# Kernel optimization log

Hardware: AMD Instinct MI355X
Metric: run time of the kernel (lower is better)

The kernel has to match this reference:

```python
import jax, jax.numpy as jnp
import numpy as np

W_SIZE = 16
WIN = 2 * W_SIZE + 1
OUT_F = 256
MODEL = 512  # output_features * 2


def setup_inputs() -> dict:
    key = jax.random.key(0)
    ks = jax.random.split(key, 7)
    B, T = 4, 2048
    s = 0.02
    return {
        "x": jax.random.normal(ks[0], (B, T, MODEL), jnp.float32),
        "encoder_outputs": jax.random.normal(ks[1], (B, T, OUT_F), jnp.float32),
        # Attention: attn Linear (OUT_F + MODEL -> OUT_F), v Linear (OUT_F -> 1, no bias)
        "W_attn": jax.random.normal(ks[2], (OUT_F + MODEL, OUT_F), jnp.float32) * s,
        "b_attn": jnp.zeros((OUT_F,), jnp.float32),
        "v": jax.random.normal(ks[3], (OUT_F,), jnp.float32) * s,
        # final linear: (MODEL + OUT_F -> OUT_F)
        "W_lin": jax.random.normal(ks[4], (MODEL + OUT_F, OUT_F), jnp.float32) * s,
        "b_lin": jnp.zeros((OUT_F,), jnp.float32),
    }


def _windows(enc):
    B, T, F = enc.shape
    padded = jnp.pad(enc, ((0, 0), (W_SIZE, W_SIZE), (0, 0)))
    idx = jnp.arange(T)[:, None] + jnp.arange(WIN)[None, :]
    return padded[:, idx]


def reference(x, encoder_outputs, W_attn, b_attn, v, W_lin, b_lin):
    win = _windows(encoder_outputs)
    B, T, W, F = win.shape
    # additive (Bahdanau) score: concat(hidden, window) -> Linear -> tanh -> v
    Wh, We = W_attn[:MODEL], W_attn[MODEL:]
    energy = jnp.tanh(
        jnp.einsum('btm,mo->bto', x, Wh)[:, :, None, :]
        + jnp.einsum('btwf,fo->btwo', win, We)
        + b_attn
    )
    scores = jnp.einsum('btwo,o->btw', energy, v)
    a = jax.nn.softmax(scores, axis=-1)
    weighted = jnp.einsum('btw,btwf->btf', a, win)        # [B, T, F]
    h = jnp.concatenate([x, weighted], axis=-1)           # [B, T, MODEL+F]
    out = jax.nn.sigmoid(jnp.einsum('btk,ko->bto', h, W_lin) + b_lin)
    return out, a[:, :, None, :]
```

## Files before the change

kernel.cpp:

```cpp
#include <hip/hip_runtime.h>
#include <math.h>

#define T_DIM 2048
#define B_DIM 4
#define BT (B_DIM * T_DIM)
#define MODEL 512
#define OUTF 256
#define WSZ 16
#define WIN 33

#define BM 128
#define BN 64
#define BK 32

#define TB 16
#define HALO 48
#define EP 264

#define ESCALE 2.885390081777927f
#define ECLAMP 30.0f

typedef __attribute__((ext_vector_type(8))) short bf16x8;
typedef __attribute__((ext_vector_type(4))) float f32x4;

__device__ inline unsigned short f2bf(float f) {
  unsigned int u = __float_as_uint(f);
  u += 0x7fffu + ((u >> 16) & 1u);
  return (unsigned short)(u >> 16);
}
__device__ inline float bflo(unsigned int u) {
  return __uint_as_float(u << 16);
}
__device__ inline float bfhi(unsigned int u) {
  return __uint_as_float(u & 0xffff0000u);
}
__device__ inline float fast_sigmoid(float z) {
  return __builtin_amdgcn_rcpf(1.f + __expf(-z));
}

__global__ __launch_bounds__(256) void prepW_kernel(
    const float* __restrict__ W_attn, const float* __restrict__ W_lin,
    unsigned short* __restrict__ wtT, unsigned short* __restrict__ wlT) {
  const int bid = blockIdx.x, o = threadIdx.x;
  const float* W = (bid < 96) ? W_attn : W_lin;
  unsigned short* WT = (bid < 96) ? wtT : wlT;
  const int k0 = ((bid < 96) ? bid : bid - 96) * 8;
  unsigned short t[8];
#pragma unroll
  for (int j = 0; j < 8; ++j) t[j] = f2bf(W[(k0 + j) * OUTF + o]);
  *(uint4*)&WT[o * 768 + k0] = *(const uint4*)t;
}

template <int KS, int MODE>
__device__ __forceinline__ void gemm_body(
    unsigned short (*As)[BM * 40], unsigned short (*Bs)[BN * 40], int rb,
    const float* __restrict__ A, int lda,
    const unsigned short* __restrict__ wtT,
    const unsigned short* __restrict__ wlT,
    const float* __restrict__ b_attn, const float* __restrict__ b_lin,
    unsigned short* __restrict__ outb, float* __restrict__ outf,
    unsigned short* __restrict__ encb) {
  const int tid = threadIdx.x;
  const int cb = rb >> 6, rp = rb & 63;
  const int row0 = rp * BM;

  const unsigned short* Bt;
  int colg;
  if (MODE == 0) {
    Bt = (cb < 4) ? (wtT + (size_t)(cb * 64) * 768)
                  : (wlT + (size_t)((cb - 4) * 64) * 768);
    colg = (cb & 3) * 64;
  } else {
    Bt = wtT + (size_t)(cb * 64) * 768 + 512;
    colg = cb * 64;
  }

  const int arow = tid >> 2, akp = (tid & 3) * 8;
  const int bcol = tid >> 3, bkp = (tid & 7) * 4;
  const float* aptr = A + (size_t)(row0 + arow) * lda + akp;
  const unsigned short* bptr = Bt + (size_t)bcol * 768 + bkp;

  float4 ra0[2], ra1[2];
  uint2 rbv[2];
  auto LOADS = [&](int sl, int ks) {
    const float* ap = aptr + ks * BK;
    ra0[sl] = *(const float4*)ap;
    ra1[sl] = *(const float4*)(ap + 4);
    rbv[sl] = *(const uint2*)(bptr + ks * BK);
  };
  auto WRITE = [&](int sl, int buf, int ks) {
    unsigned short t[8] = {f2bf(ra0[sl].x), f2bf(ra0[sl].y), f2bf(ra0[sl].z),
                           f2bf(ra0[sl].w), f2bf(ra1[sl].x), f2bf(ra1[sl].y),
                           f2bf(ra1[sl].z), f2bf(ra1[sl].w)};
    *(uint4*)&As[buf][arow * 40 + akp] = *(const uint4*)t;
    *(uint2*)&Bs[buf][bcol * 40 + bkp] = rbv[sl];
    if (MODE == 1 && cb == 0)
      *(uint4*)&encb[(size_t)(row0 + arow) * OUTF + ks * BK + akp] =
          *(const uint4*)t;
  };

  const int w = tid >> 6, lane = tid & 63;
  const int lr = lane & 15, kg = lane >> 4;
  const int rbase = (w & 3) * 32;
  const int cbase = (w >> 2) * 32;

  f32x4 acc[2][2] = {{{0.f, 0.f, 0.f, 0.f}, {0.f, 0.f, 0.f, 0.f}},
                     {{0.f, 0.f, 0.f, 0.f}, {0.f, 0.f, 0.f, 0.f}}};

  LOADS(0, 0);
  if (KS > 1) LOADS(1, 1);
  WRITE(0, 0, 0);
  __syncthreads();

#pragma unroll
  for (int ks = 0; ks < KS; ++ks) {
    if (ks + 2 < KS) LOADS(ks & 1, ks + 2);
    const int bf = ks & 1;
    bf16x8 a0 = *(const bf16x8*)&As[bf][(rbase + lr) * 40 + kg * 8];
    bf16x8 a1 = *(const bf16x8*)&As[bf][(rbase + 16 + lr) * 40 + kg * 8];
    bf16x8 b0 = *(const bf16x8*)&Bs[bf][(cbase + lr) * 40 + kg * 8];
    bf16x8 b1 = *(const bf16x8*)&Bs[bf][(cbase + 16 + lr) * 40 + kg * 8];
    acc[0][0] = __builtin_amdgcn_mfma_f32_16x16x32_bf16(a0, b0, acc[0][0], 0, 0, 0);
    acc[0][1] = __builtin_amdgcn_mfma_f32_16x16x32_bf16(a0, b1, acc[0][1], 0, 0, 0);
    acc[1][0] = __builtin_amdgcn_mfma_f32_16x16x32_bf16(a1, b0, acc[1][0], 0, 0, 0);
    acc[1][1] = __builtin_amdgcn_mfma_f32_16x16x32_bf16(a1, b1, acc[1][1], 0, 0, 0);
    if (ks + 1 < KS) WRITE((ks + 1) & 1, (ks + 1) & 1, ks + 1);
    __syncthreads();
  }

#pragma unroll
  for (int m = 0; m < 2; ++m) {
#pragma unroll
    for (int f = 0; f < 2; ++f) {
      const int col = colg + cbase + f * 16 + lr;
#pragma unroll
      for (int r = 0; r < 4; ++r) {
        const int row = row0 + rbase + m * 16 + kg * 4 + r;
        float val = acc[m][f][r];
        if (MODE == 0) {
          if (cb < 4) {
            const float y = fminf((val + b_attn[col]) * ESCALE, ECLAMP);
            outb[(size_t)row * OUTF + col] =
                f2bf(__builtin_amdgcn_exp2f(y));
          } else {
            outf[(size_t)row * OUTF + col] = val + b_lin[col];
          }
        } else {
          const float y = fminf(val * ESCALE, ECLAMP);
          outb[(size_t)row * OUTF + col] = f2bf(__builtin_amdgcn_exp2f(y));
        }
      }
    }
  }
}

__global__ __launch_bounds__(512) void gemmAB_kernel(
    const float* __restrict__ x, const float* __restrict__ enc,
    const unsigned short* __restrict__ wtT,
    const unsigned short* __restrict__ wlT,
    const float* __restrict__ b_attn, const float* __restrict__ b_lin,
    unsigned short* __restrict__ xwe2, float* __restrict__ z1,
    unsigned short* __restrict__ ewe2, unsigned short* __restrict__ encb) {
  __shared__ unsigned short As[2][BM * 40];
  __shared__ unsigned short Bs[2][BN * 40];
  if (blockIdx.x < 512)
    gemm_body<16, 0>(As, Bs, blockIdx.x, x, MODEL, wtT, wlT, b_attn, b_lin,
                     xwe2, z1, nullptr);
  else
    gemm_body<8, 1>(As, Bs, blockIdx.x - 512, enc, OUTF, wtT, wlT, nullptr,
                    nullptr, ewe2, nullptr, encb);
}

__global__ __launch_bounds__(512) void attn_gemmc_kernel(
    const unsigned short* __restrict__ xwe2,
    const unsigned short* __restrict__ ewe2,
    const unsigned short* __restrict__ encb, const float* __restrict__ v,
    const unsigned short* __restrict__ wlT, const float* __restrict__ z1,
    float* __restrict__ out, float* __restrict__ a_out) {
  __shared__ unsigned short Ew[HALO * 256];
  __shared__ unsigned short Pw[TB * EP];

  const int tid = threadIdx.x;
  const int wv = tid >> 6, lane = tid & 63;
  const int rb = ((blockIdx.x & 7) << 6) | (blockIdx.x >> 3);
  const int t0 = rb * TB;
  const int b = t0 >> 11;
  const int tloc = t0 & (T_DIM - 1);
  const int g = lane >> 4, sl = lane & 15;

  for (int u = tid; u < HALO * 32; u += 512) {
    const int r = u >> 5, s = u & 31;
    const int tg = tloc - WSZ + r;
    uint4 q;
    if ((unsigned)tg < T_DIM)
      q = *(const uint4*)(ewe2 + (((size_t)(b * T_DIM + tg)) << 8) + s * 8);
    else
      q = make_uint4(0x3f803f80u, 0x3f803f80u, 0x3f803f80u, 0x3f803f80u);
    *(uint4*)&Ew[r * 256 + s * 8] = q;
  }

  float vf[16];
  {
    const float4* vp = (const float4*)(v + sl * 16);
#pragma unroll
    for (int j = 0; j < 4; ++j) {
      float4 t4 = vp[j];
      vf[4 * j] = t4.x; vf[4 * j + 1] = t4.y;
      vf[4 * j + 2] = t4.z; vf[4 * j + 3] = t4.w;
    }
  }
  __syncthreads();

  const int lrow = wv * 2;
  const int bt0 = t0 + lrow, bt1 = bt0 + 1;

  float xe0[16], xe1[16];
  {
    const uint4* xp0 = (const uint4*)(xwe2 + ((size_t)bt0 << 8) + sl * 16);
    const uint4* xp1 = (const uint4*)(xwe2 + ((size_t)bt1 << 8) + sl * 16);
    uint4 q0 = xp0[0], q1 = xp0[1], q2 = xp1[0], q3 = xp1[1];
    unsigned int u0[8] = {q0.x, q0.y, q0.z, q0.w, q1.x, q1.y, q1.z, q1.w};
    unsigned int u1[8] = {q2.x, q2.y, q2.z, q2.w, q3.x, q3.y, q3.z, q3.w};
#pragma unroll
    for (int j = 0; j < 8; ++j) {
      xe0[2 * j] = bflo(u0[j]); xe0[2 * j + 1] = bfhi(u0[j]);
      xe1[2 * j] = bflo(u1[j]); xe1[2 * j + 1] = bfhi(u1[j]);
    }
  }

  float s0 = 0.f, s1 = 0.f;
#pragma unroll
  for (int c = 0; c < 9; ++c) {
    const int w_ = c * 4 + g;
    const int rl0 = min(lrow + w_, HALO - 1);
    const int rl1 = min(lrow + 1 + w_, HALO - 1);
    const uint4 a0q = *(const uint4*)&Ew[rl0 * 256 + sl * 16];
    const uint4 a1q = *(const uint4*)&Ew[rl0 * 256 + sl * 16 + 8];
    const uint4 b0q = *(const uint4*)&Ew[rl1 * 256 + sl * 16];
    const uint4 b1q = *(const uint4*)&Ew[rl1 * 256 + sl * 16 + 8];
    unsigned int e0[8] = {a0q.x, a0q.y, a0q.z, a0q.w, a1q.x, a1q.y, a1q.z, a1q.w};
    unsigned int e1[8] = {b0q.x, b0q.y, b0q.z, b0q.w, b1q.x, b1q.y, b1q.z, b1q.w};
    float acc0 = 0.f, acc1 = 0.f;
#pragma unroll
    for (int j = 0; j < 8; ++j) {
      const float v0 = vf[2 * j], v1 = vf[2 * j + 1];
      const float vsj = v0 + v1;
      {
        const float E0 = xe0[2 * j] * bflo(e0[j]);
        const float E1 = xe0[2 * j + 1] * bfhi(e0[j]);
        const float den = (E0 + 1.f) * (E1 + 1.f);
        float num = fmaf(v0, E1, vsj);
        num = fmaf(v1, E0, num);
        acc0 = fmaf(num, __builtin_amdgcn_rcpf(den), acc0);
      }
      {
        const float E0 = xe1[2 * j] * bflo(e1[j]);
        const float E1 = xe1[2 * j + 1] * bfhi(e1[j]);
        const float den = (E0 + 1.f) * (E1 + 1.f);
        float num = fmaf(v0, E1, vsj);
        num = fmaf(v1, E0, num);
        acc1 = fmaf(num, __builtin_amdgcn_rcpf(den), acc1);
      }
    }
#pragma unroll
    for (int off = 1; off < 16; off <<= 1) {
      acc0 += __shfl_xor(acc0, off);
      acc1 += __shfl_xor(acc1, off);
    }
    const int src = (lane & 3) << 4;
    float c0v = __shfl(acc0, src), c1v = __shfl(acc1, src);
    if ((lane >> 2) == c) { s0 = c0v; s1 = c1v; }
  }

  float p0 = (lane < WIN) ? __builtin_amdgcn_exp2f(-ESCALE * s0) : 0.f;
  float p1 = (lane < WIN) ? __builtin_amdgcn_exp2f(-ESCALE * s1) : 0.f;
  float q0 = p0, q1 = p1;
#pragma unroll
  for (int off = 1; off < 64; off <<= 1) {
    q0 += __shfl_xor(q0, off);
    q1 += __shfl_xor(q1, off);
  }
  const float a0v = p0 * __builtin_amdgcn_rcpf(q0);
  const float a1v = p1 * __builtin_amdgcn_rcpf(q1);
  if (lane < WIN) {
    a_out[(size_t)bt0 * WIN + lane] = a0v;
    a_out[(size_t)bt1 * WIN + lane] = a1v;
  }

  {
    const int o4 = lane * 4;
    const int tbase = tloc + lrow - WSZ;
    float A0 = 0.f, A1 = 0.f, A2 = 0.f, A3 = 0.f;
    float B0 = 0.f, B1 = 0.f, B2 = 0.f, B3 = 0.f;
#pragma unroll
    for (int idx = 0; idx < WIN + 1; ++idx) {
      const int t2 = tbase + idx;
      const bool valid = ((unsigned)t2 < T_DIM);
      const int t2c = valid ? t2 : 0;
      const uint2 e2 =
          *(const uint2*)(encb + (((size_t)(b * T_DIM + t2c)) << 8) + o4);
      float aw0 = __shfl(a0v, idx & 63);
      float aw1 = __shfl(a1v, (idx - 1) & 63);
      aw0 = valid ? aw0 : 0.f;
      aw1 = valid ? aw1 : 0.f;
      const float f0 = bflo(e2.x), f1 = bfhi(e2.x);
      const float f2_ = bflo(e2.y), f3 = bfhi(e2.y);
      A0 = fmaf(aw0, f0, A0); B0 = fmaf(aw1, f0, B0);
      A1 = fmaf(aw0, f1, A1); B1 = fmaf(aw1, f1, B1);
      A2 = fmaf(aw0, f2_, A2); B2 = fmaf(aw1, f2_, B2);
      A3 = fmaf(aw0, f3, A3); B3 = fmaf(aw1, f3, B3);
    }
    uint2 pk;
    pk.x = (unsigned int)f2bf(A0) | ((unsigned int)f2bf(A1) << 16);
    pk.y = (unsigned int)f2bf(A2) | ((unsigned int)f2bf(A3) << 16);
    *(uint2*)&Pw[lrow * EP + o4] = pk;
    pk.x = (unsigned int)f2bf(B0) | ((unsigned int)f2bf(B1) << 16);
    pk.y = (unsigned int)f2bf(B2) | ((unsigned int)f2bf(B3) << 16);
    *(uint2*)&Pw[(lrow + 1) * EP + o4] = pk;
  }
  __syncthreads();

  const int lr = lane & 15, kg = lane >> 4;
  f32x4 acc[2] = {{0.f, 0.f, 0.f, 0.f}, {0.f, 0.f, 0.f, 0.f}};
#pragma unroll
  for (int kk = 0; kk < 8; ++kk) {
    bf16x8 a = *(const bf16x8*)&Pw[lr * EP + kk * 32 + kg * 8];
#pragma unroll
    for (int f = 0; f < 2; ++f) {
      const unsigned short* bp =
          wlT + (size_t)(wv * 32 + f * 16 + lr) * 768 + 512 + kk * 32 + kg * 8;
      acc[f] = __builtin_amdgcn_mfma_f32_16x16x32_bf16(
          a, *(const bf16x8*)bp, acc[f], 0, 0, 0);
    }
  }
#pragma unroll
  for (int f = 0; f < 2; ++f) {
    const int col = wv * 32 + f * 16 + lr;
#pragma unroll
    for (int r = 0; r < 4; ++r) {
      const int row = t0 + kg * 4 + r;
      out[(size_t)row * OUTF + col] =
          fast_sigmoid(acc[f][r] + z1[(size_t)row * OUTF + col]);
    }
  }
}

extern "C" void kernel_launch(void* const* d_in, const int* in_sizes, int n_in,
                              void* d_out, int out_size, void* d_ws,
                              size_t ws_size, hipStream_t stream) {
  const float* x      = (const float*)d_in[0];
  const float* enc    = (const float*)d_in[1];
  const float* W_attn = (const float*)d_in[2];
  const float* b_attn = (const float*)d_in[3];
  const float* v      = (const float*)d_in[4];
  const float* W_lin  = (const float*)d_in[5];
  const float* b_lin  = (const float*)d_in[6];

  float* out   = (float*)d_out;
  float* a_out = out + (size_t)BT * OUTF;

  unsigned short* wtT  = (unsigned short*)d_ws;
  unsigned short* wlT  = wtT + 768 * OUTF;
  unsigned short* xwe2 = wlT + 768 * OUTF;
  unsigned short* ewe2 = xwe2 + (size_t)BT * OUTF;
  float*          z1   = (float*)(ewe2 + (size_t)BT * OUTF);
  unsigned short* encb = (unsigned short*)(z1 + (size_t)BT * OUTF);

  prepW_kernel<<<192, 256, 0, stream>>>(W_attn, W_lin, wtT, wlT);
  gemmAB_kernel<<<768, 512, 0, stream>>>(x, enc, wtT, wlT, b_attn, b_lin,
                                         xwe2, z1, ewe2, encb);
  attn_gemmc_kernel<<<512, 512, 0, stream>>>(xwe2, ewe2, encb, v, wlT, z1,
                                             out, a_out);
}
```

Baseline: 53.38 us.

## Precompute enc@W_lin and apply attention weights as banded MFMA over window

Result: no change. 54.02 us (+1.2%).

```diff
diff --git a/kernel.cpp b/kernel.cpp
--- a/kernel.cpp
+++ b/kernel.cpp
@@ -15,7 +15,7 @@
 
 #define TB 16
 #define HALO 48
-#define EP 264
+#define TS 72
 
 #define ESCALE 2.885390081777927f
 #define ECLAMP 30.0f
@@ -59,21 +59,19 @@
     const unsigned short* __restrict__ wlT,
     const float* __restrict__ b_attn, const float* __restrict__ b_lin,
     unsigned short* __restrict__ outb, float* __restrict__ outf,
-    unsigned short* __restrict__ encb) {
+    unsigned short* __restrict__ outb2) {
   const int tid = threadIdx.x;
   const int cb = rb >> 6, rp = rb & 63;
   const int row0 = rp * BM;
 
   const unsigned short* Bt;
-  int colg;
-  if (MODE == 0) {
+  const int colg = (cb & 3) * 64;
+  if (MODE == 0)
     Bt = (cb < 4) ? (wtT + (size_t)(cb * 64) * 768)
                   : (wlT + (size_t)((cb - 4) * 64) * 768);
-    colg = (cb & 3) * 64;
-  } else {
-    Bt = wtT + (size_t)(cb * 64) * 768 + 512;
-    colg = cb * 64;
-  }
+  else
+    Bt = (cb < 4) ? (wtT + (size_t)(cb * 64) * 768 + 512)
+                  : (wlT + (size_t)((cb - 4) * 64) * 768 + 512);
 
   const int arow = tid >> 2, akp = (tid & 3) * 8;
   const int bcol = tid >> 3, bkp = (tid & 7) * 4;
@@ -88,15 +86,12 @@
     ra1[sl] = *(const float4*)(ap + 4);
     rbv[sl] = *(const uint2*)(bptr + ks * BK);
   };
-  auto WRITE = [&](int sl, int buf, int ks) {
+  auto WRITE = [&](int sl, int buf) {
     unsigned short t[8] = {f2bf(ra0[sl].x), f2bf(ra0[sl].y), f2bf(ra0[sl].z),
                            f2bf(ra0[sl].w), f2bf(ra1[sl].x), f2bf(ra1[sl].y),
                            f2bf(ra1[sl].z), f2bf(ra1[sl].w)};
     *(uint4*)&As[buf][arow * 40 + akp] = *(const uint4*)t;
     *(uint2*)&Bs[buf][bcol * 40 + bkp] = rbv[sl];
-    if (MODE == 1 && cb == 0)
-      *(uint4*)&encb[(size_t)(row0 + arow) * OUTF + ks * BK + akp] =
-          *(const uint4*)t;
   };
 
   const int w = tid >> 6, lane = tid & 63;
@@ -109,7 +104,7 @@
 
   LOADS(0, 0);
   if (KS > 1) LOADS(1, 1);
-  WRITE(0, 0, 0);
+  WRITE(0, 0);
   __syncthreads();
 
 #pragma unroll
@@ -124,7 +119,7 @@
     acc[0][1] = __builtin_amdgcn_mfma_f32_16x16x32_bf16(a0, b1, acc[0][1], 0, 0, 0);
     acc[1][0] = __builtin_amdgcn_mfma_f32_16x16x32_bf16(a1, b0, acc[1][0], 0, 0, 0);
     acc[1][1] = __builtin_amdgcn_mfma_f32_16x16x32_bf16(a1, b1, acc[1][1], 0, 0, 0);
-    if (ks + 1 < KS) WRITE((ks + 1) & 1, (ks + 1) & 1, ks + 1);
+    if (ks + 1 < KS) WRITE((ks + 1) & 1, (ks + 1) & 1);
     __syncthreads();
   }
 
@@ -140,14 +135,17 @@
         if (MODE == 0) {
           if (cb < 4) {
             const float y = fminf((val + b_attn[col]) * ESCALE, ECLAMP);
-            outb[(size_t)row * OUTF + col] =
-                f2bf(__builtin_amdgcn_exp2f(y));
+            outb[(size_t)row * OUTF + col] = f2bf(__builtin_amdgcn_exp2f(y));
           } else {
             outf[(size_t)row * OUTF + col] = val + b_lin[col];
           }
         } else {
-          const float y = fminf(val * ESCALE, ECLAMP);
-          outb[(size_t)row * OUTF + col] = f2bf(__builtin_amdgcn_exp2f(y));
+          if (cb < 4) {
+            const float y = fminf(val * ESCALE, ECLAMP);
+            outb[(size_t)row * OUTF + col] = f2bf(__builtin_amdgcn_exp2f(y));
+          } else {
+            outb2[(size_t)row * OUTF + col] = f2bf(val);
+          }
         }
       }
     }
@@ -160,7 +158,7 @@
     const unsigned short* __restrict__ wlT,
     const float* __restrict__ b_attn, const float* __restrict__ b_lin,
     unsigned short* __restrict__ xwe2, float* __restrict__ z1,
-    unsigned short* __restrict__ ewe2, unsigned short* __restrict__ encb) {
+    unsigned short* __restrict__ ewe2, unsigned short* __restrict__ encWl2) {
   __shared__ unsigned short As[2][BM * 40];
   __shared__ unsigned short Bs[2][BN * 40];
   if (blockIdx.x < 512)
@@ -168,17 +166,18 @@
                      xwe2, z1, nullptr);
   else
     gemm_body<8, 1>(As, Bs, blockIdx.x - 512, enc, OUTF, wtT, wlT, nullptr,
-                    nullptr, ewe2, nullptr, encb);
+                    nullptr, ewe2, nullptr, encWl2);
 }
 
 __global__ __launch_bounds__(512) void attn_gemmc_kernel(
     const unsigned short* __restrict__ xwe2,
     const unsigned short* __restrict__ ewe2,
-    const unsigned short* __restrict__ encb, const float* __restrict__ v,
-    const unsigned short* __restrict__ wlT, const float* __restrict__ z1,
-    float* __restrict__ out, float* __restrict__ a_out) {
+    const unsigned short* __restrict__ encWl2, const float* __restrict__ v,
+    const float* __restrict__ z1, float* __restrict__ out,
+    float* __restrict__ a_out) {
   __shared__ unsigned short Ew[HALO * 256];
-  __shared__ unsigned short Pw[TB * EP];
+  __shared__ unsigned short EwT[256 * TS];
+  __shared__ unsigned short Ab[TB * TS];
 
   const int tid = threadIdx.x;
   const int wv = tid >> 6, lane = tid & 63;
@@ -188,15 +187,29 @@
   const int tloc = t0 & (T_DIM - 1);
   const int g = lane >> 4, sl = lane & 15;
 
+  if (tid < TB * TS / 8) ((uint4*)Ab)[tid] = make_uint4(0, 0, 0, 0);
+  {
+    const int col = tid >> 1, off = 48 + (tid & 1) * 8;
+    *(uint4*)&EwT[col * TS + off] = make_uint4(0, 0, 0, 0);
+  }
+
   for (int u = tid; u < HALO * 32; u += 512) {
     const int r = u >> 5, s = u & 31;
     const int tg = tloc - WSZ + r;
-    uint4 q;
-    if ((unsigned)tg < T_DIM)
-      q = *(const uint4*)(ewe2 + (((size_t)(b * T_DIM + tg)) << 8) + s * 8);
-    else
-      q = make_uint4(0x3f803f80u, 0x3f803f80u, 0x3f803f80u, 0x3f803f80u);
-    *(uint4*)&Ew[r * 256 + s * 8] = q;
+    uint4 qe, qw;
+    if ((unsigned)tg < T_DIM) {
+      const size_t base = ((size_t)(b * T_DIM + tg)) << 8;
+      qe = *(const uint4*)(ewe2 + base + s * 8);
+      qw = *(const uint4*)(encWl2 + base + s * 8);
+    } else {
+      qe = make_uint4(0x3f803f80u, 0x3f803f80u, 0x3f803f80u, 0x3f803f80u);
+      qw = make_uint4(0, 0, 0, 0);
+    }
+    *(uint4*)&Ew[r * 256 + s * 8] = qe;
+    unsigned short tt[8];
+    *(uint4*)tt = qw;
+#pragma unroll
+    for (int j = 0; j < 8; ++j) EwT[(s * 8 + j) * TS + r] = tt[j];
   }
 
   float vf[16];
@@ -285,52 +298,21 @@
   if (lane < WIN) {
     a_out[(size_t)bt0 * WIN + lane] = a0v;
     a_out[(size_t)bt1 * WIN + lane] = a1v;
-  }
-
-  {
-    const int o4 = lane * 4;
-    const int tbase = tloc + lrow - WSZ;
-    float A0 = 0.f, A1 = 0.f, A2 = 0.f, A3 = 0.f;
-    float B0 = 0.f, B1 = 0.f, B2 = 0.f, B3 = 0.f;
-#pragma unroll
-    for (int idx = 0; idx < WIN + 1; ++idx) {
-      const int t2 = tbase + idx;
-      const bool valid = ((unsigned)t2 < T_DIM);
-      const int t2c = valid ? t2 : 0;
-      const uint2 e2 =
-          *(const uint2*)(encb + (((size_t)(b * T_DIM + t2c)) << 8) + o4);
-      float aw0 = __shfl(a0v, idx & 63);
-      float aw1 = __shfl(a1v, (idx - 1) & 63);
-      aw0 = valid ? aw0 : 0.f;
-      aw1 = valid ? aw1 : 0.f;
-      const float f0 = bflo(e2.x), f1 = bfhi(e2.x);
-      const float f2_ = bflo(e2.y), f3 = bfhi(e2.y);
-      A0 = fmaf(aw0, f0, A0); B0 = fmaf(aw1, f0, B0);
-      A1 = fmaf(aw0, f1, A1); B1 = fmaf(aw1, f1, B1);
-      A2 = fmaf(aw0, f2_, A2); B2 = fmaf(aw1, f2_, B2);
-      A3 = fmaf(aw0, f3, A3); B3 = fmaf(aw1, f3, B3);
-    }
-    uint2 pk;
-    pk.x = (unsigned int)f2bf(A0) | ((unsigned int)f2bf(A1) << 16);
-    pk.y = (unsigned int)f2bf(A2) | ((unsigned int)f2bf(A3) << 16);
-    *(uint2*)&Pw[lrow * EP + o4] = pk;
-    pk.x = (unsigned int)f2bf(B0) | ((unsigned int)f2bf(B1) << 16);
-    pk.y = (unsigned int)f2bf(B2) | ((unsigned int)f2bf(B3) << 16);
-    *(uint2*)&Pw[(lrow + 1) * EP + o4] = pk;
+    Ab[lrow * TS + lrow + lane] = f2bf(a0v);
+    Ab[(lrow + 1) * TS + (lrow + 1) + lane] = f2bf(a1v);
   }
   __syncthreads();
 
   const int lr = lane & 15, kg = lane >> 4;
   f32x4 acc[2] = {{0.f, 0.f, 0.f, 0.f}, {0.f, 0.f, 0.f, 0.f}};
 #pragma unroll
-  for (int kk = 0; kk < 8; ++kk) {
-    bf16x8 a = *(const bf16x8*)&Pw[lr * EP + kk * 32 + kg * 8];
+  for (int ks = 0; ks < 2; ++ks) {
+    bf16x8 a = *(const bf16x8*)&Ab[lr * TS + ks * 32 + kg * 8];
 #pragma unroll
     for (int f = 0; f < 2; ++f) {
-      const unsigned short* bp =
-          wlT + (size_t)(wv * 32 + f * 16 + lr) * 768 + 512 + kk * 32 + kg * 8;
-      acc[f] = __builtin_amdgcn_mfma_f32_16x16x32_bf16(
-          a, *(const bf16x8*)bp, acc[f], 0, 0, 0);
+      bf16x8 bb = *(const bf16x8*)&EwT[(wv * 32 + f * 16 + lr) * TS +
+                                       ks * 32 + kg * 8];
+      acc[f] = __builtin_amdgcn_mfma_f32_16x16x32_bf16(a, bb, acc[f], 0, 0, 0);
     }
   }
 #pragma unroll
@@ -359,16 +341,16 @@
   float* out   = (float*)d_out;
   float* a_out = out + (size_t)BT * OUTF;
 
-  unsigned short* wtT  = (unsigned short*)d_ws;
-  unsigned short* wlT  = wtT + 768 * OUTF;
-  unsigned short* xwe2 = wlT + 768 * OUTF;
-  unsigned short* ewe2 = xwe2 + (size_t)BT * OUTF;
-  float*          z1   = (float*)(ewe2 + (size_t)BT * OUTF);
-  unsigned short* encb = (unsigned short*)(z1 + (size_t)BT * OUTF);
+  unsigned short* wtT    = (unsigned short*)d_ws;
+  unsigned short* wlT    = wtT + 768 * OUTF;
+  unsigned short* xwe2   = wlT + 768 * OUTF;
+  unsigned short* ewe2   = xwe2 + (size_t)BT * OUTF;
+  unsigned short* encWl2 = ewe2 + (size_t)BT * OUTF;
+  float*          z1     = (float*)(encWl2 + (size_t)BT * OUTF);
 
   prepW_kernel<<<192, 256, 0, stream>>>(W_attn, W_lin, wtT, wlT);
-  gemmAB_kernel<<<768, 512, 0, stream>>>(x, enc, wtT, wlT, b_attn, b_lin,
-                                         xwe2, z1, ewe2, encb);
-  attn_gemmc_kernel<<<512, 512, 0, stream>>>(xwe2, ewe2, encb, v, wlT, z1,
+  gemmAB_kernel<<<1024, 512, 0, stream>>>(x, enc, wtT, wlT, b_attn, b_lin,
+                                          xwe2, z1, ewe2, encWl2);
+  attn_gemmc_kernel<<<512, 512, 0, stream>>>(xwe2, ewe2, encWl2, v, z1,
                                              out, a_out);
 }
```
